# Performance work log

Measured on AMD Instinct MI355X. Metric: run time of the kernel, lower is better.

## Reference

```python
import jax, jax.numpy as jnp
import numpy as np

D_MODEL = 1024
NUM_HEADS = 16
HEAD_DIM = D_MODEL // NUM_HEADS
MAX_SEQ_LEN = 2048
THETA = 10000.0
BATCH = 2
SEQ = 2048


def _rope_tables():
    inv_freq = 1.0 / (THETA ** (jnp.arange(0, HEAD_DIM, 2, dtype=jnp.float32) / HEAD_DIM))
    pos = jnp.arange(MAX_SEQ_LEN, dtype=jnp.float32)
    freqs = pos[:, None] * inv_freq[None, :]  # [max_seq, head_dim/2]
    return jnp.sin(freqs), jnp.cos(freqs)


def _apply_rope(x, sin, cos):
    # x: [b, h, s, d]; sin/cos: [s, d/2] -> broadcast over b, h
    sin = sin[None, None, :, :]
    cos = cos[None, None, :, :]
    x_even = x[..., 0::2]
    x_odd = x[..., 1::2]
    out_even = x_even * cos - x_odd * sin
    out_odd = x_even * sin + x_odd * cos
    # interleave back: stack on new last axis then flatten
    out = jnp.stack((out_even, out_odd), axis=-1)
    return out.reshape(x.shape)


def setup_inputs() -> dict:
    key = jax.random.key(0)
    ks = jax.random.split(key, 5)
    std = (2.0 / (D_MODEL + D_MODEL)) ** 0.5
    return {
        "x": jax.random.normal(ks[0], (BATCH, SEQ, D_MODEL), dtype=jnp.float32),
        "Wq": jax.random.normal(ks[1], (D_MODEL, D_MODEL), dtype=jnp.float32) * std,
        "Wk": jax.random.normal(ks[2], (D_MODEL, D_MODEL), dtype=jnp.float32) * std,
        "Wv": jax.random.normal(ks[3], (D_MODEL, D_MODEL), dtype=jnp.float32) * std,
        "Wo": jax.random.normal(ks[4], (D_MODEL, D_MODEL), dtype=jnp.float32) * std,
    }


def reference(x, Wq, Wk, Wv, Wo):
    b, s, _ = x.shape
    # projections: weight stored [out, in] as in the torch Linear
    Q = jnp.einsum('bsd,od->bso', x, Wq)
    K = jnp.einsum('bsd,od->bso', x, Wk)
    V = jnp.einsum('bsd,od->bso', x, Wv)
    # split heads -> [b, h, s, hd]
    def split(t):
        return t.reshape(b, s, NUM_HEADS, HEAD_DIM).transpose(0, 2, 1, 3)
    Q, K, V = split(Q), split(K), split(V)
    sin, cos = _rope_tables()
    sin, cos = sin[:s], cos[:s]
    Q = _apply_rope(Q, sin, cos)
    K = _apply_rope(K, sin, cos)
    scale = 1.0 / jnp.sqrt(jnp.float32(HEAD_DIM))
    scores = jnp.einsum('bhqd,bhkd->bhqk', Q, K)
    causal = jnp.tril(jnp.ones((s, s), dtype=bool))[None, None]
    scores = jnp.where(causal, scores, -jnp.inf) * scale  # -inf * scale stays -inf
    attn = jax.nn.softmax(scores, axis=-1)
    out = jnp.einsum('bhqk,bhkd->bhqd', attn, V)
    out = out.transpose(0, 2, 1, 3).reshape(b, s, D_MODEL)
    return jnp.einsum('bsd,od->bso', out, Wo)
```

## Files before the change

### kernel.cpp

```cpp
#include <hip/hip_runtime.h>
#include <math.h>

#define NHEADS 16
#define HD 64
#define SEQ 2048
#define BATCH 2
#define DM 1024
#define MTOT (BATCH*SEQ)

typedef __bf16 bf16x8 __attribute__((ext_vector_type(8)));
typedef __bf16 bf16x4 __attribute__((ext_vector_type(4)));
typedef __bf16 bf16x2 __attribute__((ext_vector_type(2)));
typedef float  f32x4  __attribute__((ext_vector_type(4)));
typedef float  f32x16 __attribute__((ext_vector_type(16)));
typedef unsigned u32x4 __attribute__((ext_vector_type(4)));

#define LOG2E 1.4426950408889634f

#define GLD16(gp, lp) __builtin_amdgcn_global_load_lds( \
    (const __attribute__((address_space(1))) void*)(gp), \
    (__attribute__((address_space(3))) void*)(lp), 16, 0, 0)

__global__ __launch_bounds__(256)
void cast_all(const float* __restrict__ x, const float* __restrict__ Wq,
              const float* __restrict__ Wk, const float* __restrict__ Wv,
              const float* __restrict__ Wo,
              __bf16* __restrict__ xb, __bf16* __restrict__ Wqkvb,
              __bf16* __restrict__ Wob)
{
    const size_t NX = (size_t)MTOT * DM;
    const size_t NW_ = (size_t)DM * DM;
    const size_t i = ((size_t)blockIdx.x * 256 + threadIdx.x) * 8;
    const float* src; __bf16* dst; size_t off;
    if (i < NX)               { src = x;  dst = xb;            off = i; }
    else if (i < NX + NW_)    { src = Wq; dst = Wqkvb;         off = i - NX; }
    else if (i < NX + 2*NW_)  { src = Wk; dst = Wqkvb + NW_;   off = i - NX - NW_; }
    else if (i < NX + 3*NW_)  { src = Wv; dst = Wqkvb + 2*NW_; off = i - NX - 2*NW_; }
    else                      { src = Wo; dst = Wob;           off = i - NX - 3*NW_; }
    const float4 f0 = *(const float4*)&src[off];
    const float4 f1 = *(const float4*)&src[off + 4];
    bf16x8 o;
    o[0] = (__bf16)f0.x; o[1] = (__bf16)f0.y; o[2] = (__bf16)f0.z; o[3] = (__bf16)f0.w;
    o[4] = (__bf16)f1.x; o[5] = (__bf16)f1.y; o[6] = (__bf16)f1.z; o[7] = (__bf16)f1.w;
    *(bf16x8*)&dst[off] = o;
}

template<int BM, int BN, int MODE>
__global__ __launch_bounds__(256, 3)
void gemm_mfma(const __bf16* __restrict__ A, const __bf16* __restrict__ W,
               float* __restrict__ Cf,
               __bf16* __restrict__ Qb, __bf16* __restrict__ Kb,
               __bf16* __restrict__ Vtb)
{
    constexpr int IT = BM / 32;
    constexpr int JT = BN / 32;
    __shared__ __bf16 As[BM * 64];
    __shared__ __bf16 Bs[BN * 64];

    const int tid  = threadIdx.x;
    const int lane = tid & 63;
    const int wave = tid >> 6;
    const int ll   = lane & 15;
    const int quad = lane >> 4;
    const int wm   = (wave & 1) * (BM / 2);
    const int wn   = (wave >> 1) * (BN / 2);
    const int bm   = blockIdx.x * BM;
    const int bn   = blockIdx.y * BN;

    const __bf16* Ab = A + (size_t)bm * DM;
    const __bf16* Wb = W + (size_t)bn * DM;

    f32x4 acc[IT][JT];
#pragma unroll
    for (int i = 0; i < IT; i++)
#pragma unroll
        for (int j = 0; j < JT; j++) acc[i][j] = (f32x4){0.f, 0.f, 0.f, 0.f};

    for (int k0 = 0; k0 < DM; k0 += 64) {
#pragma unroll
        for (int j = 0; j < BM / 32; j++) {
            const int t = tid + 256 * j;
            const int r = t >> 3, g = t & 7;
            GLD16(Ab + (size_t)r * DM + k0 + ((g ^ (r & 7)) * 8), &As[t * 8]);
        }
#pragma unroll
        for (int j = 0; j < BN / 32; j++) {
            const int t = tid + 256 * j;
            const int r = t >> 3, g = t & 7;
            GLD16(Wb + (size_t)r * DM + k0 + ((g ^ (r & 7)) * 8), &Bs[t * 8]);
        }
        __syncthreads();

#pragma unroll
        for (int kh = 0; kh < 2; kh++) {
            bf16x8 af[IT], bfr[JT];
#pragma unroll
            for (int i = 0; i < IT; i++) {
                const int r = wm + i*16 + ll;
                const int g = kh*4 + quad;
                af[i] = *(const bf16x8*)&As[(r*8 + (g ^ (r & 7))) * 8];
            }
#pragma unroll
            for (int j = 0; j < JT; j++) {
                const int r = wn + j*16 + ll;
                const int g = kh*4 + quad;
                bfr[j] = *(const bf16x8*)&Bs[(r*8 + (g ^ (r & 7))) * 8];
            }
#pragma unroll
            for (int i = 0; i < IT; i++)
#pragma unroll
                for (int j = 0; j < JT; j++)
                    acc[i][j] = __builtin_amdgcn_mfma_f32_16x16x32_bf16(
                        af[i], bfr[j], acc[i][j], 0, 0, 0);
        }
        __syncthreads();
    }

    if (MODE == 1) {
#pragma unroll
        for (int i = 0; i < IT; i++) {
#pragma unroll
            for (int j = 0; j < JT; j++) {
                const int gc = bn + wn + j*16 + ll;
#pragma unroll
                for (int r = 0; r < 4; r++) {
                    const int gr = bm + wm + i*16 + quad*4 + r;
                    Cf[(size_t)gr * DM + gc] = acc[i][j][r];
                }
            }
        }
    } else {
        const int which = bn >> 10;
        const int nb = bn & 1023;
#pragma unroll
        for (int i = 0; i < IT; i++) {
            const int m0 = bm + wm + i*16 + quad*4;
            const int b  = m0 >> 11;
            const int s0 = m0 & (SEQ - 1);
#pragma unroll
            for (int j = 0; j < JT; j++) {
                const int n_g = nb + wn + j*16 + ll;
                const int h = n_g >> 6, d = n_g & (HD - 1);
                if (which == 2) {
                    bf16x4 pk;
#pragma unroll
                    for (int r = 0; r < 4; r++) pk[r] = (__bf16)acc[i][j][r];
                    *(bf16x4*)&Vtb[((size_t)((b*NHEADS + h)*HD + d)) * SEQ + s0] = pk;
                } else {
                    __bf16* P = (which == 0) ? Qb : Kb;
                    const float sc = (which == 0) ? 0.125f * LOG2E : 1.0f;
                    const float inv =
                        exp2f(-(float)(d & ~1) * (13.287712379549449f / 64.0f));
                    const bool odd = (d & 1);
#pragma unroll
                    for (int r = 0; r < 4; r++) {
                        const float own = acc[i][j][r];
                        const float oth = __shfl_xor(own, 1);
                        float sn, cs;
                        __sincosf((float)(s0 + r) * inv, &sn, &cs);
                        const float xe = odd ? oth : own;
                        const float xo = odd ? own : oth;
                        const float o = odd ? (xe * sn + xo * cs)
                                            : (xe * cs - xo * sn);
                        P[((size_t)(b*NHEADS + h) * SEQ + s0 + r) * HD + d] =
                            (__bf16)(o * sc);
                    }
                }
            }
        }
    }
}

static __device__ __forceinline__ unsigned pk2(float a, float b) {
    bf16x2 t; t[0] = (__bf16)a; t[1] = (__bf16)b;
    return __builtin_bit_cast(unsigned, t);
}

__global__ __launch_bounds__(256, 2)
void attn_mfma(const __bf16* __restrict__ Qb, const __bf16* __restrict__ Kb,
               const __bf16* __restrict__ Vtb, __bf16* __restrict__ AOb)
{
    __shared__ float comb[4][32][33];
    __shared__ float lbuf[4][2][64];

    const int tid  = threadIdx.x;
    const int wave = tid >> 6;
    const int lane = tid & 63;
    const int col  = lane & 31;
    const int hi   = lane >> 5;
    const int bh   = blockIdx.x;
    const int b    = bh >> 4, h = bh & 15;
    const int qb   = blockIdx.z ? (SEQ/64 - 1) - (int)blockIdx.y : (int)blockIdx.y;
    const int q0   = qb * 64;

    const __bf16* Qp = Qb + (size_t)bh * SEQ * HD;
    const __bf16* Kp = Kb + (size_t)bh * SEQ * HD;
    const __bf16* Vp = Vtb + (size_t)bh * HD * SEQ;

    bf16x8 qf[2][4];
#pragma unroll
    for (int i = 0; i < 2; i++)
#pragma unroll
        for (int c = 0; c < 4; c++)
            qf[i][c] = *(const bf16x8*)&Qp[(size_t)(q0 + 32*i + col) * HD
                                           + 16*c + 8*hi];

    f32x16 acc[2][2];
#pragma unroll
    for (int i = 0; i < 2; i++)
#pragma unroll
        for (int dt = 0; dt < 2; dt++) acc[i][dt] = (f32x16){};
    float lsum[2] = {0.f, 0.f};

    const int cr = col - 4*hi;

    for (int t = wave; t <= qb; t += 4) {
        const int k0 = t * 64;
        const bool diag = (t == qb);

        bf16x8 kf[2][4];
#pragma unroll
        for (int kt = 0; kt < 2; kt++)
#pragma unroll
            for (int c = 0; c < 4; c++)
                kf[kt][c] = *(const bf16x8*)&Kp[(size_t)(k0 + 32*kt + col) * HD
                                                + 16*c + 8*hi];
        bf16x4 vf[2][4][2];
#pragma unroll
        for (int dt = 0; dt < 2; dt++)
#pragma unroll
            for (int c = 0; c < 4; c++) {
                const __bf16* vrow = &Vp[(size_t)(32*dt + col) * SEQ + k0 + 16*c];
                vf[dt][c][0] = *(const bf16x4*)(vrow + 4*hi);
                vf[dt][c][1] = *(const bf16x4*)(vrow + 8 + 4*hi);
            }

#pragma unroll
        for (int i = 0; i < 2; i++) {
#pragma unroll
            for (int kt = 0; kt < 2; kt++) {
                if (kt > i && diag) continue;
                f32x16 s = (f32x16){};
#pragma unroll
                for (int c = 0; c < 4; c++)
                    s = __builtin_amdgcn_mfma_f32_32x32x16_bf16(
                        kf[kt][c], qf[i][c], s, 0, 0, 0);
                const bool tri = diag && (kt == i);
                float p[16];
#pragma unroll
                for (int r = 0; r < 16; r++) {
                    float sv = s[r];
                    if (tri && ((r & 3) + 8*(r >> 2) > cr)) sv = -INFINITY;
                    p[r] = __builtin_amdgcn_exp2f(sv);
                }
                float ls = ((p[0]+p[1])+(p[2]+p[3])) + ((p[4]+p[5])+(p[6]+p[7]))
                         + ((p[8]+p[9])+(p[10]+p[11])) + ((p[12]+p[13])+(p[14]+p[15]));
                lsum[i] += ls;
                const u32x4 w0 = {pk2(p[0],  p[1]),  pk2(p[2],  p[3]),
                                  pk2(p[4],  p[5]),  pk2(p[6],  p[7])};
                const u32x4 w1 = {pk2(p[8],  p[9]),  pk2(p[10], p[11]),
                                  pk2(p[12], p[13]), pk2(p[14], p[15])};
                const bf16x8 a0 = __builtin_bit_cast(bf16x8, w0);
                const bf16x8 a1 = __builtin_bit_cast(bf16x8, w1);
#pragma unroll
                for (int dt = 0; dt < 2; dt++) {
                    bf16x8 v0, v1;
#pragma unroll
                    for (int e = 0; e < 4; e++) {
                        v0[e]   = vf[dt][2*kt][0][e];
                        v0[4+e] = vf[dt][2*kt][1][e];
                        v1[e]   = vf[dt][2*kt+1][0][e];
                        v1[4+e] = vf[dt][2*kt+1][1][e];
                    }
                    acc[i][dt] = __builtin_amdgcn_mfma_f32_32x32x16_bf16(
                        a0, v0, acc[i][dt], 0, 0, 0);
                    acc[i][dt] = __builtin_amdgcn_mfma_f32_32x32x16_bf16(
                        a1, v1, acc[i][dt], 0, 0, 0);
                }
            }
        }
    }

#pragma unroll
    for (int i = 0; i < 2; i++)
        lbuf[wave][hi][32*i + col] = lsum[i];
    __syncthreads();

    const int qq  = tid >> 3;
    const int dd0 = (tid & 7) * 4;
#pragma unroll
    for (int i = 0; i < 2; i++) {
        float lt = 0.f;
#pragma unroll
        for (int w = 0; w < 4; w++)
            lt += lbuf[w][0][32*i + qq] + lbuf[w][1][32*i + qq];
        const float rl = 1.0f / lt;
#pragma unroll
        for (int dt = 0; dt < 2; dt++) {
#pragma unroll
            for (int r = 0; r < 16; r++)
                comb[wave][(r & 3) + 8*(r >> 2) + 4*hi][col] = acc[i][dt][r];
            __syncthreads();
            bf16x4 ov;
#pragma unroll
            for (int cc = 0; cc < 4; cc++) {
                const float o = comb[0][qq][dd0+cc] + comb[1][qq][dd0+cc]
                              + comb[2][qq][dd0+cc] + comb[3][qq][dd0+cc];
                ov[cc] = (__bf16)(o * rl);
            }
            *(bf16x4*)&AOb[(size_t)(b*SEQ + q0 + 32*i + qq) * DM
                           + h*HD + 32*dt + dd0] = ov;
            __syncthreads();
        }
    }
}

extern "C" void kernel_launch(void* const* d_in, const int* in_sizes, int n_in,
                              void* d_out, int out_size, void* d_ws, size_t ws_size,
                              hipStream_t stream) {
    const float* x  = (const float*)d_in[0];
    const float* Wq = (const float*)d_in[1];
    const float* Wk = (const float*)d_in[2];
    const float* Wv = (const float*)d_in[3];
    const float* Wo = (const float*)d_in[4];
    float* out = (float*)d_out;

    char* ws = (char*)d_ws;
    __bf16* xb    = (__bf16*)ws;
    __bf16* Wqkvb = (__bf16*)(ws + ((size_t)8  << 20));
    __bf16* Wob   = (__bf16*)(ws + ((size_t)14 << 20));
    __bf16* Qb    = (__bf16*)(ws + ((size_t)16 << 20));
    __bf16* Kb    = (__bf16*)(ws + ((size_t)24 << 20));
    __bf16* Vtb   = (__bf16*)(ws + ((size_t)32 << 20));
    __bf16* AOb   = (__bf16*)(ws + ((size_t)40 << 20));

    cast_all<<<4096, 256, 0, stream>>>(x, Wq, Wk, Wv, Wo, xb, Wqkvb, Wob);

    gemm_mfma<128,128,0><<<dim3(MTOT/128, 3072/128), 256, 0, stream>>>(
        xb, Wqkvb, nullptr, Qb, Kb, Vtb);

    attn_mfma<<<dim3(BATCH*NHEADS, SEQ/128, 2), 256, 0, stream>>>(
        Qb, Kb, Vtb, AOb);

    gemm_mfma<128,128,1><<<dim3(MTOT/128, DM/128), 256, 0, stream>>>(
        AOb, Wob, out, nullptr, nullptr, nullptr);
}
```

Baseline: 180.1 us.

## Stage K/V tiles in LDS with double-buffered async loads, 128-row query tiles

The attention kernel now assigns each wave its own 32 query rows within a 128-row query tile, and all four waves share K and V tiles. These tiles are double-buffered in LDS via global_load_lds with an XOR swizzle, replacing per-wave direct global loads and the split-K cross-wave reduction through LDS. This cuts redundant global K/V traffic and removes the combine/sync epilogue. In exchange there is a barrier per key tile, and causal imbalance across waves inside a block, since early waves skip work that later waves must do.

```diff
diff --git a/kernel.cpp b/kernel.cpp
--- a/kernel.cpp
+++ b/kernel.cpp
@@ -7,12 +7,14 @@
 #define BATCH 2
 #define DM 1024
 #define MTOT (BATCH*SEQ)
+#define QT 128
 
 typedef __bf16 bf16x8 __attribute__((ext_vector_type(8)));
 typedef __bf16 bf16x4 __attribute__((ext_vector_type(4)));
 typedef __bf16 bf16x2 __attribute__((ext_vector_type(2)));
 typedef float  f32x4  __attribute__((ext_vector_type(4)));
 typedef float  f32x16 __attribute__((ext_vector_type(16)));
+typedef unsigned u32x2 __attribute__((ext_vector_type(2)));
 typedef unsigned u32x4 __attribute__((ext_vector_type(4)));
 
 #define LOG2E 1.4426950408889634f
@@ -180,8 +182,9 @@
 void attn_mfma(const __bf16* __restrict__ Qb, const __bf16* __restrict__ Kb,
                const __bf16* __restrict__ Vtb, __bf16* __restrict__ AOb)
 {
-    __shared__ float comb[4][32][33];
-    __shared__ float lbuf[4][2][64];
+    __shared__ __align__(16) __bf16 Ks[2][64*64];
+    __shared__ __align__(16) __bf16 Vs[2][64*64];
+    __shared__ float lbuf[4][2][32];
 
     const int tid  = threadIdx.x;
     const int wave = tid >> 6;
@@ -190,127 +193,118 @@
     const int hi   = lane >> 5;
     const int bh   = blockIdx.x;
     const int b    = bh >> 4, h = bh & 15;
-    const int qb   = blockIdx.z ? (SEQ/64 - 1) - (int)blockIdx.y : (int)blockIdx.y;
-    const int q0   = qb * 64;
+    const int qb   = blockIdx.z ? (SEQ/QT - 1) - (int)blockIdx.y : (int)blockIdx.y;
+    const int q0   = qb * QT;
+    const int qw   = q0 + 32*wave;
+    const int nk   = (q0 + QT) / 64;
 
     const __bf16* Qp = Qb + (size_t)bh * SEQ * HD;
     const __bf16* Kp = Kb + (size_t)bh * SEQ * HD;
     const __bf16* Vp = Vtb + (size_t)bh * HD * SEQ;
 
-    bf16x8 qf[2][4];
-#pragma unroll
-    for (int i = 0; i < 2; i++)
-#pragma unroll
-        for (int c = 0; c < 4; c++)
-            qf[i][c] = *(const bf16x8*)&Qp[(size_t)(q0 + 32*i + col) * HD
-                                           + 16*c + 8*hi];
-
-    f32x16 acc[2][2];
-#pragma unroll
-    for (int i = 0; i < 2; i++)
-#pragma unroll
-        for (int dt = 0; dt < 2; dt++) acc[i][dt] = (f32x16){};
-    float lsum[2] = {0.f, 0.f};
-
+    bf16x8 qf[4];
+#pragma unroll
+    for (int c = 0; c < 4; c++)
+        qf[c] = *(const bf16x8*)&Qp[(size_t)(qw + col) * HD + 16*c + 8*hi];
+
+    f32x16 acc[2];
+    acc[0] = (f32x16){}; acc[1] = (f32x16){};
+    float lsum = 0.f;
     const int cr = col - 4*hi;
 
-    for (int t = wave; t <= qb; t += 4) {
-        const int k0 = t * 64;
-        const bool diag = (t == qb);
-
-        bf16x8 kf[2][4];
-#pragma unroll
-        for (int kt = 0; kt < 2; kt++)
+    {
+#pragma unroll
+        for (int j = 0; j < 2; j++) {
+            const int ti = tid + 256*j, r = ti >> 3, g = ti & 7;
+            GLD16(Kp + (size_t)r * HD + ((g ^ (r & 7)) * 8), &Ks[0][ti * 8]);
+            GLD16(Vp + (size_t)r * SEQ + ((g ^ (r & 7)) * 8), &Vs[0][ti * 8]);
+        }
+    }
+    __syncthreads();
+
+    for (int t = 0; t < nk; t++) {
+        if (t + 1 < nk) {
+            const int kn = (t + 1) * 64;
+            const int bs = (t + 1) & 1;
+#pragma unroll
+            for (int j = 0; j < 2; j++) {
+                const int ti = tid + 256*j, r = ti >> 3, g = ti & 7;
+                GLD16(Kp + (size_t)(kn + r) * HD + ((g ^ (r & 7)) * 8),
+                      &Ks[bs][ti * 8]);
+                GLD16(Vp + (size_t)r * SEQ + kn + ((g ^ (r & 7)) * 8),
+                      &Vs[bs][ti * 8]);
+            }
+        }
+
+        const __bf16* Kt = Ks[t & 1];
+        const __bf16* Vt = Vs[t & 1];
+
+#pragma unroll
+        for (int kt = 0; kt < 2; kt++) {
+            const int kb = 64*t + 32*kt;
+            if (kb > qw + 31) continue;
+
+            const int R = 32*kt + col;
+            bf16x8 kf[4];
 #pragma unroll
             for (int c = 0; c < 4; c++)
-                kf[kt][c] = *(const bf16x8*)&Kp[(size_t)(k0 + 32*kt + col) * HD
-                                                + 16*c + 8*hi];
-        bf16x4 vf[2][4][2];
-#pragma unroll
-        for (int dt = 0; dt < 2; dt++)
-#pragma unroll
-            for (int c = 0; c < 4; c++) {
-                const __bf16* vrow = &Vp[(size_t)(32*dt + col) * SEQ + k0 + 16*c];
-                vf[dt][c][0] = *(const bf16x4*)(vrow + 4*hi);
-                vf[dt][c][1] = *(const bf16x4*)(vrow + 8 + 4*hi);
-            }
-
-#pragma unroll
-        for (int i = 0; i < 2; i++) {
-#pragma unroll
-            for (int kt = 0; kt < 2; kt++) {
-                if (kt > i && diag) continue;
-                f32x16 s = (f32x16){};
-#pragma unroll
-                for (int c = 0; c < 4; c++)
-                    s = __builtin_amdgcn_mfma_f32_32x32x16_bf16(
-                        kf[kt][c], qf[i][c], s, 0, 0, 0);
-                const bool tri = diag && (kt == i);
-                float p[16];
-#pragma unroll
-                for (int r = 0; r < 16; r++) {
-                    float sv = s[r];
-                    if (tri && ((r & 3) + 8*(r >> 2) > cr)) sv = -INFINITY;
-                    p[r] = __builtin_amdgcn_exp2f(sv);
-                }
-                float ls = ((p[0]+p[1])+(p[2]+p[3])) + ((p[4]+p[5])+(p[6]+p[7]))
-                         + ((p[8]+p[9])+(p[10]+p[11])) + ((p[12]+p[13])+(p[14]+p[15]));
-                lsum[i] += ls;
-                const u32x4 w0 = {pk2(p[0],  p[1]),  pk2(p[2],  p[3]),
-                                  pk2(p[4],  p[5]),  pk2(p[6],  p[7])};
-                const u32x4 w1 = {pk2(p[8],  p[9]),  pk2(p[10], p[11]),
-                                  pk2(p[12], p[13]), pk2(p[14], p[15])};
-                const bf16x8 a0 = __builtin_bit_cast(bf16x8, w0);
-                const bf16x8 a1 = __builtin_bit_cast(bf16x8, w1);
-#pragma unroll
-                for (int dt = 0; dt < 2; dt++) {
-                    bf16x8 v0, v1;
-#pragma unroll
-                    for (int e = 0; e < 4; e++) {
-                        v0[e]   = vf[dt][2*kt][0][e];
-                        v0[4+e] = vf[dt][2*kt][1][e];
-                        v1[e]   = vf[dt][2*kt+1][0][e];
-                        v1[4+e] = vf[dt][2*kt+1][1][e];
-                    }
-                    acc[i][dt] = __builtin_amdgcn_mfma_f32_32x32x16_bf16(
-                        a0, v0, acc[i][dt], 0, 0, 0);
-                    acc[i][dt] = __builtin_amdgcn_mfma_f32_32x32x16_bf16(
-                        a1, v1, acc[i][dt], 0, 0, 0);
-                }
-            }
-        }
-    }
-
-#pragma unroll
-    for (int i = 0; i < 2; i++)
-        lbuf[wave][hi][32*i + col] = lsum[i];
+                kf[c] = *(const bf16x8*)&Kt[(R*8 + ((2*c + hi) ^ (R & 7))) * 8];
+
+            f32x16 s = (f32x16){};
+#pragma unroll
+            for (int c = 0; c < 4; c++)
+                s = __builtin_amdgcn_mfma_f32_32x32x16_bf16(
+                    kf[c], qf[c], s, 0, 0, 0);
+
+            const bool tri = (kb == qw);
+            float p[16];
+#pragma unroll
+            for (int r = 0; r < 16; r++) {
+                float sv = s[r];
+                if (tri && ((r & 3) + 8*(r >> 2) > cr)) sv = -INFINITY;
+                p[r] = __builtin_amdgcn_exp2f(sv);
+            }
+            lsum += ((p[0]+p[1])+(p[2]+p[3])) + ((p[4]+p[5])+(p[6]+p[7]))
+                  + ((p[8]+p[9])+(p[10]+p[11])) + ((p[12]+p[13])+(p[14]+p[15]));
+            const u32x4 w0 = {pk2(p[0],  p[1]),  pk2(p[2],  p[3]),
+                              pk2(p[4],  p[5]),  pk2(p[6],  p[7])};
+            const u32x4 w1 = {pk2(p[8],  p[9]),  pk2(p[10], p[11]),
+                              pk2(p[12], p[13]), pk2(p[14], p[15])};
+            const bf16x8 a0 = __builtin_bit_cast(bf16x8, w0);
+            const bf16x8 a1 = __builtin_bit_cast(bf16x8, w1);
+
+#pragma unroll
+            for (int dt = 0; dt < 2; dt++) {
+                const int R2 = 32*dt + col;
+                const int sw = R2 & 7;
+                const u32x2 g0 = *(const u32x2*)&Vt[(R2*8 + ((4*kt + 0) ^ sw)) * 8 + 4*hi];
+                const u32x2 g1 = *(const u32x2*)&Vt[(R2*8 + ((4*kt + 1) ^ sw)) * 8 + 4*hi];
+                const u32x2 g2 = *(const u32x2*)&Vt[(R2*8 + ((4*kt + 2) ^ sw)) * 8 + 4*hi];
+                const u32x2 g3 = *(const u32x2*)&Vt[(R2*8 + ((4*kt + 3) ^ sw)) * 8 + 4*hi];
+                const u32x4 vv0 = {g0.x, g0.y, g1.x, g1.y};
+                const u32x4 vv1 = {g2.x, g2.y, g3.x, g3.y};
+                const bf16x8 v0 = __builtin_bit_cast(bf16x8, vv0);
+                const bf16x8 v1 = __builtin_bit_cast(bf16x8, vv1);
+                acc[dt] = __builtin_amdgcn_mfma_f32_32x32x16_bf16(
+                    a0, v0, acc[dt], 0, 0, 0);
+                acc[dt] = __builtin_amdgcn_mfma_f32_32x32x16_bf16(
+                    a1, v1, acc[dt], 0, 0, 0);
+            }
+        }
+        __syncthreads();
+    }
+
+    lbuf[wave][hi][col] = lsum;
     __syncthreads();
 
-    const int qq  = tid >> 3;
-    const int dd0 = (tid & 7) * 4;
-#pragma unroll
-    for (int i = 0; i < 2; i++) {
-        float lt = 0.f;
-#pragma unroll
-        for (int w = 0; w < 4; w++)
-            lt += lbuf[w][0][32*i + qq] + lbuf[w][1][32*i + qq];
-        const float rl = 1.0f / lt;
-#pragma unroll
-        for (int dt = 0; dt < 2; dt++) {
-#pragma unroll
-            for (int r = 0; r < 16; r++)
-                comb[wave][(r & 3) + 8*(r >> 2) + 4*hi][col] = acc[i][dt][r];
-            __syncthreads();
-            bf16x4 ov;
-#pragma unroll
-            for (int cc = 0; cc < 4; cc++) {
-                const float o = comb[0][qq][dd0+cc] + comb[1][qq][dd0+cc]
-                              + comb[2][qq][dd0+cc] + comb[3][qq][dd0+cc];
-                ov[cc] = (__bf16)(o * rl);
-            }
-            *(bf16x4*)&AOb[(size_t)(b*SEQ + q0 + 32*i + qq) * DM
-                           + h*HD + 32*dt + dd0] = ov;
-            __syncthreads();
+#pragma unroll
+    for (int dt = 0; dt < 2; dt++) {
+#pragma unroll
+        for (int r = 0; r < 16; r++) {
+            const int row = (r & 3) + 8*(r >> 2) + 4*hi;
+            const float rl = 1.0f / (lbuf[wave][0][row] + lbuf[wave][1][row]);
+            AOb[(size_t)(b*SEQ + qw + row) * DM + h*HD + 32*dt + col] =
+                (__bf16)(acc[dt][r] * rl);
         }
     }
 }
@@ -339,7 +333,7 @@
     gemm_mfma<128,128,0><<<dim3(MTOT/128, 3072/128), 256, 0, stream>>>(
         xb, Wqkvb, nullptr, Qb, Kb, Vtb);
 
-    attn_mfma<<<dim3(BATCH*NHEADS, SEQ/128, 2), 256, 0, stream>>>(
+    attn_mfma<<<dim3(BATCH*NHEADS, SEQ/QT/2, 2), 256, 0, stream>>>(
         Qb, Kb, Vtb, AOb);
 
     gemm_mfma<128,128,1><<<dim3(MTOT/128, DM/128), 256, 0, stream>>>(
```

Result: faster. 174.4 us (-3.2%).
